# Optimization experiments

Hardware: AMD Instinct MI355X
Metric: run time of the kernel (lower is better)

The kernel has to match this reference:

```python
import jax, jax.numpy as jnp
import numpy as np

N = 50000    # nodes
E = 800000   # edges per relation
R = 3        # relations
IN, HID, OUT = 128, 128, 64


def setup_inputs() -> dict:
    key = jax.random.key(0)
    ks = jax.random.split(key, 7)
    x = jax.random.normal(ks[0], (N, IN), jnp.float32)
    src = jax.random.randint(ks[1], (R, E), 0, N)
    dst = jax.random.randint(ks[2], (R, E), 0, N)
    W1 = jax.random.normal(ks[3], (R, IN, HID), jnp.float32) / np.sqrt(IN)
    b1 = jnp.zeros((R, HID), jnp.float32)
    W2 = jax.random.normal(ks[4], (R, HID, OUT), jnp.float32) / np.sqrt(HID)
    b2 = jnp.zeros((R, OUT), jnp.float32)
    return {"x": x, "src": src, "dst": dst, "W1": W1, "b1": b1, "W2": W2, "b2": b2}


def _rel_conv(x, src, dst, W, b):
    """dgl GraphConv with norm='both' and self-loops added (dgl.add_self_loop).
    out = D_dst^{-1/2} A_sl (D_src^{-1/2} X W) + b  (weight order commutes)."""
    loop = jnp.arange(N, dtype=src.dtype)
    s = jnp.concatenate([src, loop])  # [E+N] self-loops appended
    d = jnp.concatenate([dst, loop])
    ones = jnp.ones(s.shape[0], x.dtype)
    deg_out = jax.ops.segment_sum(ones, s, num_segments=N)  # >= 1 due to self loops
    deg_in = jax.ops.segment_sum(ones, d, num_segments=N)
    h = (x * jax.lax.rsqrt(deg_out)[:, None]) @ W          # [N, F_out]
    agg = jax.ops.segment_sum(h[s], d, num_segments=N)     # gather-scatter SpMM
    return agg * jax.lax.rsqrt(deg_in)[:, None] + b


def _hetero_layer(x, src, dst, W, b):
    # HeteroGraphConv with aggregate='sum': sum per-relation GraphConv outputs.
    out = _rel_conv(x, src[0], dst[0], W[0], b[0])
    for r in range(1, R):  # small fixed relation count
        out = out + _rel_conv(x, src[r], dst[r], W[r], b[r])
    return out


def reference(x, src, dst, W1, b1, W2, b2):
    h = jax.nn.relu(_hetero_layer(x, src, dst, W1, b1))
    return _hetero_layer(h, src, dst, W2, b2)
```

## Files before the change

### kernel.cpp

```cpp
#include <hip/hip_runtime.h>
#include <hip/hip_fp16.h>


constexpr int N   = 50000;
constexpr int R   = 3;
constexpr int IN  = 128;
constexpr int HID = 128;
constexpr int OUT = 64;
constexpr int M   = R * N;
constexpr int BK  = 1024;
constexpr int NBKT = (M + BK - 1) / BK;
constexpr int CHUNK = 8192;
constexpr int KB  = 24;
constexpr int CVT_N4 = N * IN / 4;
constexpr int WPK   = 6 * KB * 64;
constexpr int WPK_B = (WPK + 255) / 256;
constexpr int NPASS = 4;
constexpr int QC    = IN / NPASS;

typedef _Float16 half8 __attribute__((ext_vector_type(8)));
typedef float floatx16 __attribute__((ext_vector_type(16)));

__global__ void prep_kernel(const float* __restrict__ x,
                            const float* __restrict__ W1, const float* __restrict__ W2,
                            const float* __restrict__ b1, const float* __restrict__ b2,
                            __half* __restrict__ x16,
                            __half* __restrict__ F1, __half* __restrict__ F2,
                            float* __restrict__ bsum1, float* __restrict__ bsum2) {
    int b = blockIdx.x;
    if (b == 0) {
        int t = threadIdx.x;
        if (t < HID) bsum1[t] = b1[t] + b1[HID + t] + b1[2 * HID + t];
        if (t < OUT) bsum2[t] = b2[t] + b2[OUT + t] + b2[2 * OUT + t];
        return;
    }
    if (b <= WPK_B) {
        int idx = (b - 1) * 256 + threadIdx.x;
        if (idx < 4 * KB * 64) {
            int nt = idx / (KB * 64), rem = idx % (KB * 64);
            int kb = rem / 64, lane = rem % 64;
            int c = nt * 32 + (lane & 31);
            int k0 = kb * 16 + (lane >> 5) * 8;
            __half h[8];
#pragma unroll
            for (int j = 0; j < 8; j++) h[j] = __float2half_rn(W1[(k0 + j) * 128 + c]);
            *(uint4*)(F1 + (size_t)idx * 8) = *(uint4*)h;
        } else if (idx < 6 * KB * 64) {
            int i2 = idx - 4 * KB * 64;
            int nt = i2 / (KB * 64), rem = i2 % (KB * 64);
            int kb = rem / 64, lane = rem % 64;
            int c = nt * 32 + (lane & 31);
            int k0 = kb * 16 + (lane >> 5) * 8;
            __half h[8];
#pragma unroll
            for (int j = 0; j < 8; j++) h[j] = __float2half_rn(W2[(k0 + j) * 64 + c]);
            *(uint4*)(F2 + (size_t)i2 * 8) = *(uint4*)h;
        }
        return;
    }
    int i = (b - 1 - WPK_B) * 256 + threadIdx.x;
    if (i >= CVT_N4) return;
    float4 v = ((const float4*)x)[i];
    __half2 a = __floats2half2_rn(v.x, v.y);
    __half2 c = __floats2half2_rn(v.z, v.w);
    uint2 o;
    o.x = *(unsigned*)&a;
    o.y = *(unsigned*)&c;
    int n  = i >> 5;
    int c4 = (i & 31) * 4;
    int q  = c4 >> 5;
    int cq = c4 & 31;
    *(uint2*)(x16 + (size_t)q * N * QC + (size_t)n * QC + cq) = o;
}

__global__ __launch_bounds__(256) void p1_kernel(const int* __restrict__ src,
                                                 const int* __restrict__ dst,
                                                 int E, int RE, int nb,
                                                 int* __restrict__ bh) {
    __shared__ int hd[NBKT], hs[NBKT];
    for (int i = threadIdx.x; i < NBKT; i += 256) { hd[i] = 0; hs[i] = 0; }
    __syncthreads();
    int beg = blockIdx.x * CHUNK, end = min(RE, beg + CHUNK);
    for (int g = beg + (int)threadIdx.x; g < end; g += 256) {
        int rb = ((g >= E) + (g >= 2 * E)) * N;
        atomicAdd(&hd[(rb + dst[g]) >> 10], 1);
        atomicAdd(&hs[(rb + src[g]) >> 10], 1);
    }
    __syncthreads();
    for (int i = threadIdx.x; i < NBKT; i += 256) {
        bh[i * nb + blockIdx.x] = hd[i];
        bh[(NBKT + i) * nb + blockIdx.x] = hs[i];
    }
}

__global__ void scan1_kernel(const int* __restrict__ in, int* __restrict__ out,
                             int* __restrict__ partials, int L) {
    __shared__ int lds[1024];
    int t = threadIdx.x;
    int idx = blockIdx.x * 1024 + t;
    int v = (idx < L) ? in[idx] : 0;
    lds[t] = v;
    __syncthreads();
    for (int off = 1; off < 1024; off <<= 1) {
        int u = (t >= off) ? lds[t - off] : 0;
        __syncthreads();
        lds[t] += u;
        __syncthreads();
    }
    if (idx < L) out[idx] = lds[t] - v;
    if (t == 1023) partials[blockIdx.x] = lds[1023];
}

__global__ void scan2_kernel(int* __restrict__ partials, int nb1) {
    __shared__ int lds[256];
    int t = threadIdx.x;
    int v = (t < nb1) ? partials[t] : 0;
    lds[t] = v;
    __syncthreads();
    for (int off = 1; off < 256; off <<= 1) {
        int u = (t >= off) ? lds[t - off] : 0;
        __syncthreads();
        lds[t] += u;
        __syncthreads();
    }
    if (t < nb1) partials[t] = lds[t] - v;
}

__global__ __launch_bounds__(256) void p3_kernel(const int* __restrict__ src,
                                                 const int* __restrict__ dst,
                                                 int E, int RE, int nb,
                                                 const int* __restrict__ scanv,
                                                 const int* __restrict__ partials,
                                                 int* __restrict__ ebd,
                                                 unsigned short* __restrict__ ebs) {
    __shared__ int cd[NBKT], cs[NBKT];
    for (int i = threadIdx.x; i < NBKT; i += 256) {
        int id = i * nb + blockIdx.x;
        int is = (NBKT + i) * nb + blockIdx.x;
        cd[i] = scanv[id] + partials[id >> 10];
        cs[i] = scanv[is] + partials[is >> 10] - RE;
    }
    __syncthreads();
    int beg = blockIdx.x * CHUNK, end = min(RE, beg + CHUNK);
    for (int g = beg + (int)threadIdx.x; g < end; g += 256) {
        int rb = ((g >= E) + (g >= 2 * E)) * N;
        int s  = src[g];
        int kd = rb + dst[g];
        int pd = atomicAdd(&cd[kd >> 10], 1);
        ebd[pd] = (s << 10) | (kd & 1023);
        int ks = rb + s;
        int ps = atomicAdd(&cs[ks >> 10], 1);
        ebs[ps] = (unsigned short)(ks & 1023);
    }
}

__global__ __launch_bounds__(1024) void pbs_kernel(const int* __restrict__ scanv,
                                                   const int* __restrict__ partials,
                                                   int nb, int RE,
                                                   const unsigned short* __restrict__ ebs,
                                                   float* __restrict__ rs_out) {
    __shared__ int cnt[BK];
    int t = threadIdx.x;
    int k = blockIdx.x;
    int i0 = (NBKT + k) * nb;
    int segbeg = scanv[i0] + partials[i0 >> 10] - RE;
    int segend;
    if (k == NBKT - 1) segend = RE;
    else {
        int i1 = i0 + nb;
        segend = scanv[i1] + partials[i1 >> 10] - RE;
    }
    cnt[t] = 0;
    __syncthreads();
    for (int e = segbeg + t; e < segend; e += 1024)
        atomicAdd(&cnt[(int)ebs[e]], 1);
    __syncthreads();
    int slot = k * BK + t;
    if (slot < M) rs_out[slot] = rsqrtf((float)(cnt[t] + 1));
}

__global__ __launch_bounds__(1024) void pbd_kernel(const int* __restrict__ scanv,
                                                   const int* __restrict__ partials,
                                                   int nb, int RE,
                                                   const int* __restrict__ ebd,
                                                   const float* __restrict__ rs_out,
                                                   int* __restrict__ row_ptr,
                                                   float* __restrict__ rs_in,
                                                   unsigned int* __restrict__ esrc) {
    __shared__ int cnt[BK];
    __shared__ int cur[BK];
    int t = threadIdx.x;
    int k = blockIdx.x;
    int i0 = k * nb;
    int segbeg = scanv[i0] + partials[i0 >> 10];
    int segend;
    if (k == NBKT - 1) segend = RE;
    else {
        int i1 = (k + 1) * nb;
        segend = scanv[i1] + partials[i1 >> 10];
    }
    cnt[t] = 0;
    __syncthreads();
    for (int e = segbeg + t; e < segend; e += 1024)
        atomicAdd(&cnt[ebd[e] & 1023], 1);
    __syncthreads();
    int slot = k * BK + t;
    int c = cnt[t];
    cur[t] = c;
    __syncthreads();
    for (int off = 1; off < 1024; off <<= 1) {
        int u = (t >= off) ? cur[t - off] : 0;
        __syncthreads();
        cur[t] += u;
        __syncthreads();
    }
    int excl = cur[t] - c;
    if (slot < M) {
        row_ptr[slot] = segbeg + excl;
        rs_in[slot] = rsqrtf((float)(c + 1));
    }
    if (k == NBKT - 1 && t == 0) row_ptr[M] = RE;
    __syncthreads();
    cur[t] = segbeg + excl;
    __syncthreads();
    for (int e = segbeg + t; e < segend; e += 1024) {
        int v = ebd[e];
        int key = k * BK + (v & 1023);
        int r = (key >= 2 * N) + (key >= N);
        unsigned s = (unsigned)(v >> 10);
        int pos = atomicAdd(&cur[v & 1023], 1);
        __half h = __float2half_rn(rs_out[r * N + s]);
        esrc[pos] = s | ((unsigned)__half_as_ushort(h) << 16);
    }
}

__global__ __launch_bounds__(256) void gather_kernel(const __half* __restrict__ Xh,
                                                     const float* __restrict__ rs_in,
                                                     const float* __restrict__ rs_out,
                                                     const int* __restrict__ row_ptr,
                                                     const unsigned int* __restrict__ esrc,
                                                     __half* __restrict__ Z16) {
    int q = blockIdx.y;
    int lane = threadIdx.x & 63;
    int wv = threadIdx.x >> 6;
    int g = lane >> 3;
    int cl = lane & 7;
    int n = blockIdx.x * 32 + wv * 8 + g;
    bool valid = (n < N);
    int nc = valid ? n : 0;
    const __half* Xq = Xh + (size_t)q * N * QC;
    uint2 xn = *(const uint2*)(Xq + (long)nc * QC + cl * 4);
    const __half2 z2 = __float2half2_rn(0.f);
#pragma unroll
    for (int r = 0; r < R; r++) {
        int key = r * N + nc;
        int beg = row_ptr[key];
        int end = valid ? row_ptr[key + 1] : beg;
        __half2 acc0 = z2, acc1 = z2;
        for (int e = beg; __any(e < end); e += 8) {
            unsigned u[8];
#pragma unroll
            for (int i = 0; i < 8; i++)
                u[i] = (e + i < end) ? esrc[e + i] : 0u;
            uint2 y[8];
#pragma unroll
            for (int i = 0; i < 8; i++)
                y[i] = *(const uint2*)(Xq + (long)(u[i] & 0xffffu) * QC + cl * 4);
#pragma unroll
            for (int i = 0; i < 8; i++) {
                __half2 cc = __half2half2(__ushort_as_half((unsigned short)(u[i] >> 16)));
                acc0 = __hfma2(*(__half2*)&y[i].x, cc, acc0);
                acc1 = __hfma2(*(__half2*)&y[i].y, cc, acc1);
            }
        }
        __half2 cs = __float2half2_rn(rs_out[key]);
        acc0 = __hfma2(*(__half2*)&xn.x, cs, acc0);
        acc1 = __hfma2(*(__half2*)&xn.y, cs, acc1);
        __half2 ri = __float2half2_rn(rs_in[key]);
        acc0 = __hmul2(acc0, ri);
        acc1 = __hmul2(acc1, ri);
        if (valid) {
            uint2 o;
            o.x = *(unsigned*)&acc0;
            o.y = *(unsigned*)&acc1;
            *(uint2*)(Z16 + (long)n * 384 + r * 128 + q * QC + cl * 4) = o;
        }
    }
}

__global__ __launch_bounds__(256) void mfma_gemm1_kernel(const __half* __restrict__ Z16,
                                                         const __half* __restrict__ F,
                                                         const float* __restrict__ bias,
                                                         __half* __restrict__ H16) {
    int wave = threadIdx.x >> 6, lane = threadIdx.x & 63;
    int m0 = blockIdx.x * 128 + wave * 32;
    int mr = min(m0 + (lane & 31), N - 1);
    const half8* A = (const half8*)(Z16 + (long)mr * 384 + (lane >> 5) * 8);
    const half8* B = (const half8*)F;
    floatx16 acc[4];
#pragma unroll
    for (int i = 0; i < 4; i++)
#pragma unroll
        for (int j = 0; j < 16; j++) acc[i][j] = 0.f;

    half8 a = A[0];
    for (int kb = 0; kb < KB; kb++) {
        half8 an = (kb < KB - 1) ? A[(kb + 1) * 2] : a;
#pragma unroll
        for (int nt = 0; nt < 4; nt++) {
            half8 b = B[(nt * KB + kb) * 64 + lane];
            acc[nt] = __builtin_amdgcn_mfma_f32_32x32x16_f16(a, b, acc[nt], 0, 0, 0);
        }
        a = an;
    }
    float bv[4];
#pragma unroll
    for (int nt = 0; nt < 4; nt++) bv[nt] = bias[nt * 32 + (lane & 31)];
    int rbase = m0 + 4 * (lane >> 5);
    int col0 = lane & 31;
#pragma unroll
    for (int nt = 0; nt < 4; nt++) {
#pragma unroll
        for (int reg = 0; reg < 16; reg++) {
            int row = rbase + (reg & 3) + 8 * (reg >> 2);
            if (row < N) {
                float v = fmaxf(acc[nt][reg] + bv[nt], 0.f);
                H16[(long)row * 128 + nt * 32 + col0] = __float2half_rn(v);
            }
        }
    }
}

__global__ __launch_bounds__(256) void mfma_gemmY_kernel(const __half* __restrict__ H16,
                                                         const __half* __restrict__ F,
                                                         __half* __restrict__ Y2) {
    int wave = threadIdx.x >> 6, lane = threadIdx.x & 63;
    int r = blockIdx.y;
    int m0 = blockIdx.x * 128 + wave * 32;
    int mr = min(m0 + (lane & 31), N - 1);
    const half8* A = (const half8*)(H16 + (long)mr * 128 + (lane >> 5) * 8);
    const half8* B = (const half8*)F;
    floatx16 acc[2];
#pragma unroll
    for (int i = 0; i < 2; i++)
#pragma unroll
        for (int j = 0; j < 16; j++) acc[i][j] = 0.f;

#pragma unroll
    for (int kbr = 0; kbr < 8; kbr++) {
        half8 a = A[kbr * 2];
#pragma unroll
        for (int nt = 0; nt < 2; nt++) {
            half8 b = B[(nt * KB + r * 8 + kbr) * 64 + lane];
            acc[nt] = __builtin_amdgcn_mfma_f32_32x32x16_f16(a, b, acc[nt], 0, 0, 0);
        }
    }
    int rbase = m0 + 4 * (lane >> 5);
    int col0 = lane & 31;
    __half* Yr = Y2 + (long)r * N * 64;
#pragma unroll
    for (int nt = 0; nt < 2; nt++) {
#pragma unroll
        for (int reg = 0; reg < 16; reg++) {
            int row = rbase + (reg & 3) + 8 * (reg >> 2);
            if (row < N)
                Yr[(long)row * 64 + nt * 32 + col0] = __float2half_rn(acc[nt][reg]);
        }
    }
}

__global__ __launch_bounds__(256) void gather_out_kernel(const __half* __restrict__ Y2,
                                                         const float* __restrict__ rs_in,
                                                         const float* __restrict__ rs_out,
                                                         const int* __restrict__ row_ptr,
                                                         const unsigned int* __restrict__ esrc,
                                                         const float* __restrict__ bias,
                                                         float* __restrict__ outp) {
    int n = blockIdx.x * 4 + (threadIdx.x >> 6);
    if (n >= N) return;
    int lane = threadIdx.x & 63;
    int pair = lane >> 5;
    int c2 = (lane & 31) * 2;
    const __half2 z2 = __float2half2_rn(0.f);
    float2 tot = ((const float2*)bias)[lane & 31];
#pragma unroll
    for (int r = 0; r < R; r++) {
        int key = r * N + n;
        const __half* Yr = Y2 + (long)r * N * 64;
        __half2 acc = z2;
        int beg = row_ptr[key], end = row_ptr[key + 1];
        int e = beg;
        for (; e + 16 <= end; e += 16) {
            unsigned u[8];
            __half2 y[8];
#pragma unroll
            for (int j = 0; j < 8; j++) u[j] = esrc[e + 2 * j + pair];
#pragma unroll
            for (int j = 0; j < 8; j++)
                y[j] = *(const __half2*)(Yr + (long)(u[j] & 0xffffu) * 64 + c2);
#pragma unroll
            for (int j = 0; j < 8; j++)
                acc = __hfma2(y[j], __half2half2(__ushort_as_half((unsigned short)(u[j] >> 16))), acc);
        }
        for (; e + 8 <= end; e += 8) {
            unsigned u[4];
            __half2 y[4];
#pragma unroll
            for (int j = 0; j < 4; j++) u[j] = esrc[e + 2 * j + pair];
#pragma unroll
            for (int j = 0; j < 4; j++)
                y[j] = *(const __half2*)(Yr + (long)(u[j] & 0xffffu) * 64 + c2);
#pragma unroll
            for (int j = 0; j < 4; j++)
                acc = __hfma2(y[j], __half2half2(__ushort_as_half((unsigned short)(u[j] >> 16))), acc);
        }
        for (; e < end; e += 2) {
            int idx = e + pair;
            unsigned u = (idx < end) ? esrc[idx] : 0u;
            __half2 y = *(const __half2*)(Yr + (long)(u & 0xffffu) * 64 + c2);
            acc = __hfma2(y, __half2half2(__ushort_as_half((unsigned short)(u >> 16))), acc);
        }
        unsigned a0 = *(unsigned*)&acc;
        unsigned b0 = (unsigned)__shfl_xor((int)a0, 32, 64);
        acc = __hadd2(acc, *(__half2*)&b0);
        __half2 ys = *(const __half2*)(Yr + (long)n * 64 + c2);
        acc = __hfma2(ys, __float2half2_rn(rs_out[key]), acc);
        float2 f = __half22float2(acc);
        float ri = rs_in[key];
        tot.x += ri * f.x;
        tot.y += ri * f.y;
    }
    if (pair == 0) *(float2*)(outp + (long)n * 64 + c2) = tot;
}

extern "C" void kernel_launch(void* const* d_in, const int* in_sizes, int n_in,
                              void* d_out, int out_size, void* d_ws, size_t ws_size,
                              hipStream_t stream) {
    const float* x  = (const float*)d_in[0];
    const int*  src = (const int*)d_in[1];
    const int*  dst = (const int*)d_in[2];
    const float* W1 = (const float*)d_in[3];
    const float* b1 = (const float*)d_in[4];
    const float* W2 = (const float*)d_in[5];
    const float* b2 = (const float*)d_in[6];
    float* out = (float*)d_out;
    const int E  = in_sizes[1] / R;
    const int RE = in_sizes[1];
    const int nb = (RE + CHUNK - 1) / CHUNK;
    const int L  = 2 * NBKT * nb;
    const int nb1 = (L + 1023) / 1024;

    char* ws = (char*)d_ws;
    size_t off = 0;
    auto alloc = [&](size_t bytes) -> void* {
        void* p = ws + off;
        off += (bytes + 255) & ~(size_t)255;
        return p;
    };
    float* bsum1    = (float*)alloc(HID * 4);
    float* bsum2    = (float*)alloc(OUT * 4);
    float* rs_in    = (float*)alloc((size_t)M * 4);
    float* rs_out   = (float*)alloc((size_t)M * 4);
    int*   row_ptr  = (int*)alloc((size_t)(M + 1) * 4);
    int*   bh       = (int*)alloc((size_t)L * 4);
    int*   scanv    = (int*)alloc((size_t)L * 4);
    int*   partials = (int*)alloc((size_t)nb1 * 4);
    unsigned* esrc  = (unsigned*)alloc((size_t)RE * 4);
    __half* F1      = (__half*)alloc((size_t)4 * KB * 64 * 8 * 2);
    __half* F2      = (__half*)alloc((size_t)2 * KB * 64 * 8 * 2);
    char*  regA     = (char*)alloc((size_t)N * 384 * 2);
    int*   ebd      = (int*)regA;
    unsigned short* ebs = (unsigned short*)(regA + (size_t)RE * 4);
    __half* Z16     = (__half*)regA;
    __half* Y2      = (__half*)regA;
    __half* x16     = (__half*)alloc((size_t)N * IN * 2);
    __half* H16     = (__half*)alloc((size_t)N * HID * 2);

    prep_kernel<<<1 + WPK_B + (CVT_N4 + 255) / 256, 256, 0, stream>>>(
        x, W1, W2, b1, b2, x16, F1, F2, bsum1, bsum2);
    p1_kernel<<<nb, 256, 0, stream>>>(src, dst, E, RE, nb, bh);
    scan1_kernel<<<nb1, 1024, 0, stream>>>(bh, scanv, partials, L);
    scan2_kernel<<<1, 256, 0, stream>>>(partials, nb1);
    p3_kernel<<<nb, 256, 0, stream>>>(src, dst, E, RE, nb, scanv, partials, ebd, ebs);
    pbs_kernel<<<NBKT, 1024, 0, stream>>>(scanv, partials, nb, RE, ebs, rs_out);
    pbd_kernel<<<NBKT, 1024, 0, stream>>>(scanv, partials, nb, RE, ebd, rs_out,
                                          row_ptr, rs_in, esrc);

    const int ab  = (N + 3) / 4;
    const int gb1 = (N + 31) / 32;
    const int ggb = (N + 127) / 128;

    gather_kernel<<<dim3(gb1, NPASS), 256, 0, stream>>>(x16, rs_in, rs_out, row_ptr,
                                                        esrc, Z16);
    mfma_gemm1_kernel<<<ggb, 256, 0, stream>>>(Z16, F1, bsum1, H16);
    mfma_gemmY_kernel<<<dim3(ggb, R), 256, 0, stream>>>(H16, F2, Y2);
    gather_out_kernel<<<ab, 256, 0, stream>>>(Y2, rs_in, rs_out, row_ptr, esrc,
                                              bsum2, out);
}
```

Baseline: 380.2 us.

## Aggregate before transform in layer two and reuse the chunked gather kernel

Layer two now gathers the 128-wide hidden features per relation, reusing the layer-one gather kernel, and then runs a single GEMM from 384 to 64 with bias, writing fp32 output directly. This replaces the old per-relation Y GEMM and the separate 64-wide output gather. GEMM1 now writes H in a column-chunked layout so each gather pass reads a compact 32-column slab. The gather kernel is also reworked to 16 lanes per node with 4-byte loads, and each column chunk is a separate launch. The trade-off is that the layer-two gather moves about twice as many feature bytes per edge, in exchange for fewer kernels and smaller per-pass working sets.

Measured after the change: 430.6 us. 13.3% more time.

```diff
diff --git a/kernel.cpp b/kernel.cpp
--- a/kernel.cpp
+++ b/kernel.cpp
@@ -234,64 +234,51 @@
     }
 }
 
-__global__ __launch_bounds__(256) void gather_kernel(const __half* __restrict__ Xh,
+__global__ __launch_bounds__(256) void gather_kernel(const __half* __restrict__ Xq,
                                                      const float* __restrict__ rs_in,
                                                      const float* __restrict__ rs_out,
                                                      const int* __restrict__ row_ptr,
                                                      const unsigned int* __restrict__ esrc,
-                                                     __half* __restrict__ Z16) {
-    int q = blockIdx.y;
+                                                     __half* __restrict__ Zq) {
     int lane = threadIdx.x & 63;
     int wv = threadIdx.x >> 6;
-    int g = lane >> 3;
-    int cl = lane & 7;
-    int n = blockIdx.x * 32 + wv * 8 + g;
-    bool valid = (n < N);
-    int nc = valid ? n : 0;
-    const __half* Xq = Xh + (size_t)q * N * QC;
-    uint2 xn = *(const uint2*)(Xq + (long)nc * QC + cl * 4);
+    int g = lane >> 4;
+    int cl = lane & 15;
+    int n = blockIdx.x * 16 + wv * 4 + g;
+    unsigned xn = *(const unsigned*)(Xq + (long)n * QC + cl * 2);
     const __half2 z2 = __float2half2_rn(0.f);
 #pragma unroll
     for (int r = 0; r < R; r++) {
-        int key = r * N + nc;
-        int beg = row_ptr[key];
-        int end = valid ? row_ptr[key + 1] : beg;
-        __half2 acc0 = z2, acc1 = z2;
-        for (int e = beg; __any(e < end); e += 8) {
+        int key = r * N + n;
+        int beg = row_ptr[key], end = row_ptr[key + 1];
+        __half2 acc = z2;
+        for (int e = beg; e < end; e += 8) {
             unsigned u[8];
 #pragma unroll
             for (int i = 0; i < 8; i++)
                 u[i] = (e + i < end) ? esrc[e + i] : 0u;
-            uint2 y[8];
+            unsigned y[8];
 #pragma unroll
             for (int i = 0; i < 8; i++)
-                y[i] = *(const uint2*)(Xq + (long)(u[i] & 0xffffu) * QC + cl * 4);
+                y[i] = *(const unsigned*)(Xq + (long)(u[i] & 0xffffu) * QC + cl * 2);
 #pragma unroll
             for (int i = 0; i < 8; i++) {
                 __half2 cc = __half2half2(__ushort_as_half((unsigned short)(u[i] >> 16)));
-                acc0 = __hfma2(*(__half2*)&y[i].x, cc, acc0);
-                acc1 = __hfma2(*(__half2*)&y[i].y, cc, acc1);
+                acc = __hfma2(*(__half2*)&y[i], cc, acc);
             }
         }
         __half2 cs = __float2half2_rn(rs_out[key]);
-        acc0 = __hfma2(*(__half2*)&xn.x, cs, acc0);
-        acc1 = __hfma2(*(__half2*)&xn.y, cs, acc1);
+        acc = __hfma2(*(__half2*)&xn, cs, acc);
         __half2 ri = __float2half2_rn(rs_in[key]);
-        acc0 = __hmul2(acc0, ri);
-        acc1 = __hmul2(acc1, ri);
-        if (valid) {
-            uint2 o;
-            o.x = *(unsigned*)&acc0;
-            o.y = *(unsigned*)&acc1;
-            *(uint2*)(Z16 + (long)n * 384 + r * 128 + q * QC + cl * 4) = o;
-        }
+        acc = __hmul2(acc, ri);
+        *(unsigned*)(Zq + (long)n * 384 + r * 128 + cl * 2) = *(unsigned*)&acc;
     }
 }
 
 __global__ __launch_bounds__(256) void mfma_gemm1_kernel(const __half* __restrict__ Z16,
                                                          const __half* __restrict__ F,
                                                          const float* __restrict__ bias,
-                                                         __half* __restrict__ H16) {
+                                                         __half* __restrict__ H16p) {
     int wave = threadIdx.x >> 6, lane = threadIdx.x & 63;
     int m0 = blockIdx.x * 128 + wave * 32;
     int mr = min(m0 + (lane & 31), N - 1);
@@ -325,20 +312,20 @@
             int row = rbase + (reg & 3) + 8 * (reg >> 2);
             if (row < N) {
                 float v = fmaxf(acc[nt][reg] + bv[nt], 0.f);
-                H16[(long)row * 128 + nt * 32 + col0] = __float2half_rn(v);
+                H16p[(size_t)nt * N * 32 + (long)row * 32 + col0] = __float2half_rn(v);
             }
         }
     }
 }
 
-__global__ __launch_bounds__(256) void mfma_gemmY_kernel(const __half* __restrict__ H16,
+__global__ __launch_bounds__(256) void mfma_gemm2_kernel(const __half* __restrict__ Z16,
                                                          const __half* __restrict__ F,
-                                                         __half* __restrict__ Y2) {
+                                                         const float* __restrict__ bias,
+                                                         float* __restrict__ outp) {
     int wave = threadIdx.x >> 6, lane = threadIdx.x & 63;
-    int r = blockIdx.y;
     int m0 = blockIdx.x * 128 + wave * 32;
     int mr = min(m0 + (lane & 31), N - 1);
-    const half8* A = (const half8*)(H16 + (long)mr * 128 + (lane >> 5) * 8);
+    const half8* A = (const half8*)(Z16 + (long)mr * 384 + (lane >> 5) * 8);
     const half8* B = (const half8*)F;
     floatx16 acc[2];
 #pragma unroll
@@ -346,91 +333,30 @@
 #pragma unroll
         for (int j = 0; j < 16; j++) acc[i][j] = 0.f;
 
-#pragma unroll
-    for (int kbr = 0; kbr < 8; kbr++) {
-        half8 a = A[kbr * 2];
+    half8 a = A[0];
+    for (int kb = 0; kb < KB; kb++) {
+        half8 an = (kb < KB - 1) ? A[(kb + 1) * 2] : a;
 #pragma unroll
         for (int nt = 0; nt < 2; nt++) {
-            half8 b = B[(nt * KB + r * 8 + kbr) * 64 + lane];
+            half8 b = B[(nt * KB + kb) * 64 + lane];
             acc[nt] = __builtin_amdgcn_mfma_f32_32x32x16_f16(a, b, acc[nt], 0, 0, 0);
         }
-    }
+        a = an;
+    }
+    float bv[2];
+#pragma unroll
+    for (int nt = 0; nt < 2; nt++) bv[nt] = bias[nt * 32 + (lane & 31)];
     int rbase = m0 + 4 * (lane >> 5);
     int col0 = lane & 31;
-    __half* Yr = Y2 + (long)r * N * 64;
 #pragma unroll
     for (int nt = 0; nt < 2; nt++) {
 #pragma unroll
         for (int reg = 0; reg < 16; reg++) {
             int row = rbase + (reg & 3) + 8 * (reg >> 2);
             if (row < N)
-                Yr[(long)row * 64 + nt * 32 + col0] = __float2half_rn(acc[nt][reg]);
-        }
-    }
-}
-
-__global__ __launch_bounds__(256) void gather_out_kernel(const __half* __restrict__ Y2,
-                                                         const float* __restrict__ rs_in,
-                                                         const float* __restrict__ rs_out,
-                                                         const int* __restrict__ row_ptr,
-                                                         const unsigned int* __restrict__ esrc,
-                                                         const float* __restrict__ bias,
-                                                         float* __restrict__ outp) {
-    int n = blockIdx.x * 4 + (threadIdx.x >> 6);
-    if (n >= N) return;
-    int lane = threadIdx.x & 63;
-    int pair = lane >> 5;
-    int c2 = (lane & 31) * 2;
-    const __half2 z2 = __float2half2_rn(0.f);
-    float2 tot = ((const float2*)bias)[lane & 31];
-#pragma unroll
-    for (int r = 0; r < R; r++) {
-        int key = r * N + n;
-        const __half* Yr = Y2 + (long)r * N * 64;
-        __half2 acc = z2;
-        int beg = row_ptr[key], end = row_ptr[key + 1];
-        int e = beg;
-        for (; e + 16 <= end; e += 16) {
-            unsigned u[8];
-            __half2 y[8];
-#pragma unroll
-            for (int j = 0; j < 8; j++) u[j] = esrc[e + 2 * j + pair];
-#pragma unroll
-            for (int j = 0; j < 8; j++)
-                y[j] = *(const __half2*)(Yr + (long)(u[j] & 0xffffu) * 64 + c2);
-#pragma unroll
-            for (int j = 0; j < 8; j++)
-                acc = __hfma2(y[j], __half2half2(__ushort_as_half((unsigned short)(u[j] >> 16))), acc);
-        }
-        for (; e + 8 <= end; e += 8) {
-            unsigned u[4];
-            __half2 y[4];
-#pragma unroll
-            for (int j = 0; j < 4; j++) u[j] = esrc[e + 2 * j + pair];
-#pragma unroll
-            for (int j = 0; j < 4; j++)
-                y[j] = *(const __half2*)(Yr + (long)(u[j] & 0xffffu) * 64 + c2);
-#pragma unroll
-            for (int j = 0; j < 4; j++)
-                acc = __hfma2(y[j], __half2half2(__ushort_as_half((unsigned short)(u[j] >> 16))), acc);
-        }
-        for (; e < end; e += 2) {
-            int idx = e + pair;
-            unsigned u = (idx < end) ? esrc[idx] : 0u;
-            __half2 y = *(const __half2*)(Yr + (long)(u & 0xffffu) * 64 + c2);
-            acc = __hfma2(y, __half2half2(__ushort_as_half((unsigned short)(u >> 16))), acc);
-        }
-        unsigned a0 = *(unsigned*)&acc;
-        unsigned b0 = (unsigned)__shfl_xor((int)a0, 32, 64);
-        acc = __hadd2(acc, *(__half2*)&b0);
-        __half2 ys = *(const __half2*)(Yr + (long)n * 64 + c2);
-        acc = __hfma2(ys, __float2half2_rn(rs_out[key]), acc);
-        float2 f = __half22float2(acc);
-        float ri = rs_in[key];
-        tot.x += ri * f.x;
-        tot.y += ri * f.y;
-    }
-    if (pair == 0) *(float2*)(outp + (long)n * 64 + c2) = tot;
+                outp[(long)row * 64 + nt * 32 + col0] = acc[nt][reg] + bv[nt];
+        }
+    }
 }
 
 extern "C" void kernel_launch(void* const* d_in, const int* in_sizes, int n_in,
@@ -472,9 +398,8 @@
     int*   ebd      = (int*)regA;
     unsigned short* ebs = (unsigned short*)(regA + (size_t)RE * 4);
     __half* Z16     = (__half*)regA;
-    __half* Y2      = (__half*)regA;
     __half* x16     = (__half*)alloc((size_t)N * IN * 2);
-    __half* H16     = (__half*)alloc((size_t)N * HID * 2);
+    __half* H16p    = (__half*)alloc((size_t)N * HID * 2);
 
     prep_kernel<<<1 + WPK_B + (CVT_N4 + 255) / 256, 256, 0, stream>>>(
         x, W1, W2, b1, b2, x16, F1, F2, bsum1, bsum2);
@@ -486,14 +411,17 @@
     pbd_kernel<<<NBKT, 1024, 0, stream>>>(scanv, partials, nb, RE, ebd, rs_out,
                                           row_ptr, rs_in, esrc);
 
-    const int ab  = (N + 3) / 4;
-    const int gb1 = (N + 31) / 32;
+    const int gb  = N / 16;
     const int ggb = (N + 127) / 128;
 
-    gather_kernel<<<dim3(gb1, NPASS), 256, 0, stream>>>(x16, rs_in, rs_out, row_ptr,
-                                                        esrc, Z16);
-    mfma_gemm1_kernel<<<ggb, 256, 0, stream>>>(Z16, F1, bsum1, H16);
-    mfma_gemmY_kernel<<<dim3(ggb, R), 256, 0, stream>>>(H16, F2, Y2);
-    gather_out_kernel<<<ab, 256, 0, stream>>>(Y2, rs_in, rs_out, row_ptr, esrc,
-                                              bsum2, out);
-}
+    for (int q = 0; q < NPASS; q++)
+        gather_kernel<<<gb, 256, 0, stream>>>(x16 + (size_t)q * N * QC, rs_in,
+                                              rs_out, row_ptr, esrc,
+                                              Z16 + (size_t)q * QC);
+    mfma_gemm1_kernel<<<ggb, 256, 0, stream>>>(Z16, F1, bsum1, H16p);
+    for (int q = 0; q < NPASS; q++)
+        gather_kernel<<<gb, 256, 0, stream>>>(H16p + (size_t)q * N * QC, rs_in,
+                                              rs_out, row_ptr, esrc,
+                                              Z16 + (size_t)q * QC);
+    mfma_gemm2_kernel<<<ggb, 256, 0, stream>>>(Z16, F2, bsum2, out);
+}
```
